# Optimization experiments

Measured on AMD Instinct MI355X. Metric: run time of the kernel, lower is better.

The kernel has to match this reference:

```python
import jax, jax.numpy as jnp
import numpy as np

N = 65536   # query points
M = 65536   # support points
H = 32      # neighbors per query
IN = 64     # input feature dim
OUT = 64    # out_dim // 2
K = 15      # kernel points
EXTENT = 0.1 * 1.2 / 2.5  # radius * kp_extent / conv_radius = 0.048
BN_EPS = 1e-5


def setup_inputs() -> dict:
    key = jax.random.key(0)
    ks = jax.random.split(key, 8)
    x = jax.random.normal(ks[0], (M, IN), dtype=jnp.float32)
    q_pts = jax.random.uniform(ks[1], (N, 3), dtype=jnp.float32) * 0.1
    s_pts = jax.random.uniform(ks[2], (M, 3), dtype=jnp.float32) * 0.1
    neighb_inds = jax.random.randint(ks[3], (N, H), 0, M, dtype=jnp.int32)
    kernel_points = jax.random.normal(ks[4], (K, 3), dtype=jnp.float32) * (0.5 * EXTENT)
    weights = jax.random.normal(ks[5], (K, IN, OUT), dtype=jnp.float32) * 0.05
    gamma = jnp.ones((OUT,), dtype=jnp.float32)
    beta = jnp.zeros((OUT,), dtype=jnp.float32)
    return {"x": x, "q_pts": q_pts, "s_pts": s_pts, "neighb_inds": neighb_inds,
            "kernel_points": kernel_points, "weights": weights,
            "gamma": gamma, "beta": beta}


def reference(x, q_pts, s_pts, neighb_inds, kernel_points, weights, gamma, beta):
    # --- KPConv (rigid, linear influence, sum aggregation) ---
    # Shadow point/feature for out-of-range neighbor indices (KPConv convention).
    s_pad = jnp.concatenate([s_pts, jnp.full((1, 3), 1e6, s_pts.dtype)], axis=0)
    x_pad = jnp.concatenate([x, jnp.zeros((1, x.shape[1]), x.dtype)], axis=0)

    # Relative neighbor coordinates: [N, H, 3]
    neighbors = s_pad[neighb_inds] - q_pts[:, None, :]
    # Squared distance to each kernel point: [N, H, K]
    diffs = neighbors[:, :, None, :] - kernel_points[None, None, :, :]
    sq_dist = jnp.sum(diffs * diffs, axis=-1)
    # Linear kernel-point influence, clipped at 0: [N, H, K]
    all_weights = jnp.maximum(1.0 - jnp.sqrt(sq_dist) / EXTENT, 0.0)

    # Gather neighbor features: [N, H, IN]
    neighb_x = x_pad[neighb_inds]
    # Influence-weighted aggregation per kernel point: [N, K, IN]
    weighted = jnp.einsum('nhk,nhi->nki', all_weights, neighb_x)
    # Apply per-kernel-point weight matrices and sum over kernel points: [N, OUT]
    out = jnp.einsum('nki,kio->no', weighted, weights)

    # --- BatchNorm (training-mode statistics over points) ---
    mean = jnp.mean(out, axis=0)
    var = jnp.var(out, axis=0)
    out = (out - mean) / jnp.sqrt(var + BN_EPS) * gamma + beta

    # --- LeakyReLU(0.1) ---
    return jnp.where(out >= 0, out, 0.1 * out)
```

## Files before the change

### kernel.cpp

```cpp
#include <hip/hip_runtime.h>
#include <math.h>

#define NQ   65536
#define H    32
#define IN   64
#define OUTC 64
#define K    15
#define QB   16
#define INV_EXT (1.0f / 0.048f)

#define OFF_PSUM  131072
#define OFF_SCSH  (OFF_PSUM + 2097152)
#define OFF_XBF   (OFF_SCSH + 1024)
#define NEED_BF16 (OFF_XBF + (size_t)NQ * IN * 2)

typedef __attribute__((ext_vector_type(8))) short short8;
typedef __attribute__((ext_vector_type(4))) short short4v;
typedef __attribute__((ext_vector_type(4))) float float4v;

static __device__ __forceinline__ unsigned short f2bf(float f) {
    return (unsigned short)((__float_as_uint(f) + 0x8000u) >> 16);
}
static __device__ __forceinline__ unsigned pk2(float a, float b) {
    return (__float_as_uint(a) + 0x8000u) >> 16 |
           ((__float_as_uint(b) + 0x8000u) & 0xFFFF0000u);
}

__global__ __launch_bounds__(256) void prep_all(
    const float* __restrict__ W, const float* __restrict__ x,
    short* __restrict__ Bfrag, unsigned short* __restrict__ xbf, int do_x)
{
    const int b = blockIdx.x;
    if (b < 4096) {
        if (do_x) {
            const int t = b * 256 + threadIdx.x;
            const float4 v = ((const float4*)x)[t];
            uint2 p; p.x = pk2(v.x, v.y); p.y = pk2(v.z, v.w);
            ((uint2*)xbf)[t] = p;
        }
    } else {
        const int t2  = (b - 4096) * 256 + threadIdx.x;
        const int j   = t2 & 7;
        const int ln  = (t2 >> 3) & 63;
        const int tt  = (t2 >> 9) & 31;
        const int wvq = t2 >> 14;
        const int kp2 = tt * 32 + (ln >> 4) * 8 + j;
        const int kq  = kp2 & 15;
        const int ii  = kp2 >> 4;
        const int oo  = wvq * 16 + (ln & 15);
        const float val = (kq < K) ? W[(kq * 64 + ii) * 64 + oo] : 0.0f;
        Bfrag[t2] = (short)f2bf(val);
    }
}

template<bool BFX>
__global__ __launch_bounds__(256, 5) void kpconv_mfma(
    const float* __restrict__ x, const unsigned short* __restrict__ xbf,
    const float* __restrict__ qp, const float* __restrict__ sp,
    const int* __restrict__ inds, const float* __restrict__ kp,
    const short* __restrict__ Bfrag, float* __restrict__ out_raw,
    float* __restrict__ psum)
{
    __shared__ __align__(16) short lds[16384];
    short* xn  = lds;
    short* wT2 = lds + 8448;

    const int tid  = threadIdx.x;
    const int lane = tid & 63;
    const int wv   = tid >> 6;
    const int quad = lane >> 4;
    const int ml   = lane & 15;
    const int q8   = lane >> 3;
    const int m8   = lane & 7;
    const int q0   = blockIdx.x * QB;

    short* xn_own = xn + wv * 2112;

    short8  xv[4][4];
    float4v xf[4][4][2];
#pragma unroll
    for (int qi = 0; qi < 4; ++qi) {
        const int ibase = (q0 + wv * 4 + qi) * H;
#pragma unroll
        for (int j = 0; j < 4; ++j) {
            const int id = inds[ibase + j * 8 + q8];
            if (BFX) {
                xv[qi][j] = *(const short8*)((const short*)xbf + id * IN + m8 * 8);
            } else {
                xf[qi][j][0] = *(const float4v*)(x + id * IN + m8 * 8);
                xf[qi][j][1] = *(const float4v*)(x + id * IN + m8 * 8 + 4);
            }
        }
    }

#pragma unroll
    for (int rep = 0; rep < 2; ++rep) {
        const int p  = lane + rep * 64;
        const int qi = p >> 5, h = p & 31;
        const int qg = wv * 4 + qi;
        const int n  = q0 + qg;
        const int id = inds[n * H + h];
        const float dx = sp[id * 3 + 0] - qp[n * 3 + 0];
        const float dy = sp[id * 3 + 1] - qp[n * 3 + 1];
        const float dz = sp[id * 3 + 2] - qp[n * 3 + 2];
        short8 w0, w1;
#pragma unroll
        for (int k = 0; k < K; ++k) {
            const float ex = dx - kp[k * 3 + 0];
            const float ey = dy - kp[k * 3 + 1];
            const float ez = dz - kp[k * 3 + 2];
            const float sq = ex * ex + ey * ey + ez * ez;
            float wval = 1.0f - __builtin_amdgcn_sqrtf(sq) * INV_EXT;
            wval = wval > 0.0f ? wval : 0.0f;
            if (k < 8) w0[k]     = (short)f2bf(wval);
            else       w1[k - 8] = (short)f2bf(wval);
        }
        w1[7] = 0;
        short* dst = wT2 + qg * 512 + ((h >> 2) & 1) * 256 + (h >> 3) * 64 + (h & 3) * 16;
        *(short8*)dst       = w0;
        *(short8*)(dst + 8) = w1;
    }

#pragma unroll
    for (int qi = 0; qi < 3; ++qi)
#pragma unroll
        for (int j = 0; j < 4; ++j) {
            if (BFX) {
                asm volatile("" :: "v"(xv[qi][j]));
            } else {
                asm volatile("" :: "v"(xf[qi][j][0]));
                asm volatile("" :: "v"(xf[qi][j][1]));
            }
        }

    const unsigned ldsb = (unsigned)(size_t)(&lds[0]);
    const unsigned xnb  = ldsb + (unsigned)(wv * 4224 + lane * 8);
    const unsigned wtb  = ldsb + 16896u + (unsigned)(wv * 4096 + lane * 8);

    float4v frag[4][4];
#pragma unroll
    for (int qi = 0; qi < 4; ++qi)
#pragma unroll
        for (int v = 0; v < 4; ++v) frag[qi][v] = (float4v){0.f, 0.f, 0.f, 0.f};

    const int Eb = (m8 >> 1) * 528 + ((q8 >> 2) & 1) * 256 + (q8 & 3) * 16 + (m8 & 1) * 8;

#pragma unroll
    for (int qi = 0; qi < 4; ++qi) {
#pragma unroll
        for (int j = 0; j < 4; ++j) {
            short8 pv;
            if (BFX) {
                pv = xv[qi][j];
            } else {
                const float4v a0 = xf[qi][j][0], a1 = xf[qi][j][1];
                pv[0] = (short)f2bf(a0[0]); pv[1] = (short)f2bf(a0[1]);
                pv[2] = (short)f2bf(a0[2]); pv[3] = (short)f2bf(a0[3]);
                pv[4] = (short)f2bf(a1[0]); pv[5] = (short)f2bf(a1[1]);
                pv[6] = (short)f2bf(a1[2]); pv[7] = (short)f2bf(a1[3]);
            }
            *(short8*)&xn_own[Eb + j * 64] = pv;
        }
        __builtin_amdgcn_sched_barrier(0);

        short4v a0, a1, b0[4], b1[4];
        asm volatile("ds_read_b64_tr_b16 %0, %1 offset:%c2"
                     : "=v"(a0) : "v"(wtb), "i"(qi * 1024) : "memory");
        asm volatile("ds_read_b64_tr_b16 %0, %1 offset:%c2"
                     : "=v"(a1) : "v"(wtb), "i"(qi * 1024 + 512) : "memory");
#pragma unroll
        for (int v = 0; v < 4; ++v) {
            asm volatile("ds_read_b64_tr_b16 %0, %1 offset:%c2"
                         : "=v"(b0[v]) : "v"(xnb), "i"(v * 1056) : "memory");
            asm volatile("ds_read_b64_tr_b16 %0, %1 offset:%c2"
                         : "=v"(b1[v]) : "v"(xnb), "i"(v * 1056 + 512) : "memory");
        }
        asm volatile("s_waitcnt lgkmcnt(0)");
        __builtin_amdgcn_sched_barrier(0);

        short8 a;
#pragma unroll
        for (int e = 0; e < 4; ++e) { a[e] = a0[e]; a[e + 4] = a1[e]; }
#pragma unroll
        for (int v = 0; v < 4; ++v) {
            short8 bb;
#pragma unroll
            for (int e = 0; e < 4; ++e) { bb[e] = b0[v][e]; bb[e + 4] = b1[v][e]; }
            frag[qi][v] = __builtin_amdgcn_mfma_f32_16x16x32_bf16(a, bb, frag[qi][v], 0, 0, 0);
        }
    }

    __syncthreads();

    char* AwtB = (char*)lds;
#pragma unroll
    for (int qi = 0; qi < 4; ++qi) {
        const int qg = wv * 4 + qi;
        char* qb = AwtB + qg * 2048;
        const int xr = ((qg & 7) << 4) ^ (((qg >> 3) & 1) << 3) ^ ((ml >> 2) << 3);
#pragma unroll
        for (int v = 0; v < 4; ++v) {
            short4v w;
#pragma unroll
            for (int r = 0; r < 4; ++r) w[r] = (short)f2bf(frag[qi][v][r]);
            const int Bw = (v * 16 + ml) * 32 + quad * 8;
            *(short4v*)(qb + (Bw ^ xr)) = w;
        }
    }
    __syncthreads();

    float4v acc0 = (float4v){0.f, 0.f, 0.f, 0.f};
    float4v acc1 = (float4v){0.f, 0.f, 0.f, 0.f};
    const short* bptr = Bfrag + (wv * 32) * 512 + lane * 8;
    const char*  arow = AwtB + ml * 2048;
    const int    xr2  = ((ml & 7) << 4) ^ (((ml >> 3) & 1) << 3);
#pragma unroll 2
    for (int t = 0; t < 32; t += 2) {
        {
            const int Br = t * 64 + quad * 16;
            const int ad = Br ^ xr2 ^ (((t >> 1) & 3) << 3);
            const short4v alo = *(const short4v*)(arow + ad);
            const short4v ahi = *(const short4v*)(arow + (ad ^ 8));
            short8 a;
#pragma unroll
            for (int e = 0; e < 4; ++e) { a[e] = alo[e]; a[e + 4] = ahi[e]; }
            const short8 bb = *(const short8*)(bptr + t * 512);
            acc0 = __builtin_amdgcn_mfma_f32_16x16x32_bf16(a, bb, acc0, 0, 0, 0);
        }
        {
            const int t1 = t + 1;
            const int Br = t1 * 64 + quad * 16;
            const int ad = Br ^ xr2 ^ (((t1 >> 1) & 3) << 3);
            const short4v alo = *(const short4v*)(arow + ad);
            const short4v ahi = *(const short4v*)(arow + (ad ^ 8));
            short8 a;
#pragma unroll
            for (int e = 0; e < 4; ++e) { a[e] = alo[e]; a[e + 4] = ahi[e]; }
            const short8 bb = *(const short8*)(bptr + t1 * 512);
            acc1 = __builtin_amdgcn_mfma_f32_16x16x32_bf16(a, bb, acc1, 0, 0, 0);
        }
    }
    const float4v acc = acc0 + acc1;

    float s = 0.f, s2 = 0.f;
#pragma unroll
    for (int r = 0; r < 4; ++r) {
        const float v = acc[r];
        out_raw[(q0 + quad * 4 + r) * OUTC + wv * 16 + ml] = v;
        s += v; s2 += v * v;
    }
    s  += __shfl_xor(s, 16, 64);  s  += __shfl_xor(s, 32, 64);
    s2 += __shfl_xor(s2, 16, 64); s2 += __shfl_xor(s2, 32, 64);
    if (quad == 0) {
        const int c = wv * 16 + ml;
        psum[c * 4096 + blockIdx.x]          = s;
        psum[262144 + c * 4096 + blockIdx.x] = s2;
    }
}

__global__ __launch_bounds__(256) void bn_stats(
    const float* __restrict__ psum, const float* __restrict__ gamma,
    const float* __restrict__ beta, float* __restrict__ sc_sh)
{
    const int c = blockIdx.x;
    const int t = threadIdx.x;
    float s = 0.f, q = 0.f;
#pragma unroll
    for (int i = 0; i < 16; ++i) {
        s += psum[c * 4096 + t + i * 256];
        q += psum[262144 + c * 4096 + t + i * 256];
    }
    __shared__ float rs[4], rq[4];
#pragma unroll
    for (int off = 32; off; off >>= 1) {
        s += __shfl_down(s, off, 64);
        q += __shfl_down(q, off, 64);
    }
    if ((t & 63) == 0) { rs[t >> 6] = s; rq[t >> 6] = q; }
    __syncthreads();
    if (t == 0) {
        s = rs[0] + rs[1] + rs[2] + rs[3];
        q = rq[0] + rq[1] + rq[2] + rq[3];
        const float mean = s * (1.0f / (float)NQ);
        const float var  = q * (1.0f / (float)NQ) - mean * mean;
        const float scale = gamma[c] / sqrtf(var + 1e-5f);
        sc_sh[c]      = scale;
        sc_sh[64 + c] = beta[c] - mean * scale;
    }
}

__global__ __launch_bounds__(256) void bn_apply(
    float* __restrict__ out, const float* __restrict__ sc_sh)
{
    __shared__ float sc[64];
    __shared__ float sh[64];
    if (threadIdx.x < 64) {
        sc[threadIdx.x] = sc_sh[threadIdx.x];
        sh[threadIdx.x] = sc_sh[64 + threadIdx.x];
    }
    __syncthreads();
    const int idx = blockIdx.x * 256 + threadIdx.x;
#pragma unroll
    for (int it = 0; it < 4; ++it) {
        const int e = idx + it * 262144;
        float4 v = ((const float4*)out)[e];
        const int cg = (e & 15) * 4;
        float4 r;
        r.x = v.x * sc[cg + 0] + sh[cg + 0];
        r.y = v.y * sc[cg + 1] + sh[cg + 1];
        r.z = v.z * sc[cg + 2] + sh[cg + 2];
        r.w = v.w * sc[cg + 3] + sh[cg + 3];
        r.x = r.x >= 0.0f ? r.x : 0.1f * r.x;
        r.y = r.y >= 0.0f ? r.y : 0.1f * r.y;
        r.z = r.z >= 0.0f ? r.z : 0.1f * r.z;
        r.w = r.w >= 0.0f ? r.w : 0.1f * r.w;
        ((float4*)out)[e] = r;
    }
}

extern "C" void kernel_launch(void* const* d_in, const int* in_sizes, int n_in,
                              void* d_out, int out_size, void* d_ws, size_t ws_size,
                              hipStream_t stream)
{
    (void)in_sizes; (void)n_in; (void)out_size;
    const float* x     = (const float*)d_in[0];
    const float* qp    = (const float*)d_in[1];
    const float* sp    = (const float*)d_in[2];
    const int*   inds  = (const int*)d_in[3];
    const float* kp    = (const float*)d_in[4];
    const float* W     = (const float*)d_in[5];
    const float* gamma = (const float*)d_in[6];
    const float* beta  = (const float*)d_in[7];
    float* out = (float*)d_out;

    short*          Bfrag = (short*)d_ws;
    float*          psum  = (float*)((char*)d_ws + OFF_PSUM);
    float*          sc_sh = (float*)((char*)d_ws + OFF_SCSH);
    unsigned short* xbf   = (unsigned short*)((char*)d_ws + OFF_XBF);

    const int use_bf = (ws_size >= NEED_BF16) ? 1 : 0;

    prep_all<<<4352, 256, 0, stream>>>(W, x, Bfrag, xbf, use_bf);
    if (use_bf)
        kpconv_mfma<true><<<NQ / QB, 256, 0, stream>>>(x, xbf, qp, sp, inds, kp, Bfrag, out, psum);
    else
        kpconv_mfma<false><<<NQ / QB, 256, 0, stream>>>(x, xbf, qp, sp, inds, kp, Bfrag, out, psum);
    bn_stats<<<64, 256, 0, stream>>>(psum, gamma, beta, sc_sh);
    bn_apply<<<1024, 256, 0, stream>>>(out, sc_sh);
}
```

Baseline: 145.5 us.

## Fuse prep, KPConv, BN stats and BN apply into one cooperative persistent kernel

Replaces the four-launch pipeline (prep, kpconv, bn_stats, bn_apply) with a single cooperative kernel. It runs the weight and feature prep, grid-syncs, loops persistently over query tiles accumulating per-thread BN sums, reduces them with atomics, grid-syncs again and then applies BN plus LeakyReLU. The goal is to remove launch gaps and the separate partial-sum pass. The costs are grid-wide barriers, a persistent grid limited by occupancy with fewer blocks than tiles, and atomic float accumulation of the statistics. If the cooperative launch fails, the code falls back to the old path.

New measurement: 366.2 us. 152% more time.

```diff
diff --git a/kernel.cpp b/kernel.cpp
--- a/kernel.cpp
+++ b/kernel.cpp
@@ -1,5 +1,8 @@
 #include <hip/hip_runtime.h>
+#include <hip/hip_cooperative_groups.h>
 #include <math.h>
+
+namespace cg = cooperative_groups;
 
 #define NQ   65536
 #define H    32
@@ -7,6 +10,7 @@
 #define OUTC 64
 #define K    15
 #define QB   16
+#define NTILE 4096
 #define INV_EXT (1.0f / 0.048f)
 
 #define OFF_PSUM  131072
@@ -24,6 +28,271 @@
 static __device__ __forceinline__ unsigned pk2(float a, float b) {
     return (__float_as_uint(a) + 0x8000u) >> 16 |
            ((__float_as_uint(b) + 0x8000u) & 0xFFFF0000u);
+}
+
+template<bool BFX>
+__global__ __launch_bounds__(256, 4) void kpconv_fused(
+    const float* __restrict__ x, unsigned short* __restrict__ xbf,
+    const float* __restrict__ qp, const float* __restrict__ sp,
+    const int* __restrict__ inds, const float* __restrict__ kp,
+    short* __restrict__ Bfrag, const float* __restrict__ W,
+    const float* __restrict__ gamma, const float* __restrict__ beta,
+    float* __restrict__ out, float* __restrict__ gsum)
+{
+    __shared__ __align__(16) short lds[16384];
+    short* xn  = lds;
+    short* wT2 = lds + 8448;
+
+    const int tid  = threadIdx.x;
+    const int lane = tid & 63;
+    const int wv   = tid >> 6;
+    const int quad = lane >> 4;
+    const int ml   = lane & 15;
+    const int q8   = lane >> 3;
+    const int m8   = lane & 7;
+    const int G    = gridDim.x;
+
+    if (blockIdx.x < 256) {
+        const int t2  = blockIdx.x * 256 + tid;
+        const int j   = t2 & 7;
+        const int ln  = (t2 >> 3) & 63;
+        const int tt  = (t2 >> 9) & 31;
+        const int wvq = t2 >> 14;
+        const int kp2 = tt * 32 + (ln >> 4) * 8 + j;
+        const int kq  = kp2 & 15;
+        const int ii  = kp2 >> 4;
+        const int oo  = wvq * 16 + (ln & 15);
+        const float val = (kq < K) ? W[(kq * 64 + ii) * 64 + oo] : 0.0f;
+        Bfrag[t2] = (short)f2bf(val);
+    }
+    if (BFX) {
+        for (unsigned t = blockIdx.x * 256u + tid; t < 1048576u; t += (unsigned)G * 256u) {
+            const float4 v = ((const float4*)x)[t];
+            uint2 p; p.x = pk2(v.x, v.y); p.y = pk2(v.z, v.w);
+            ((uint2*)xbf)[t] = p;
+        }
+    }
+    if (blockIdx.x == 0 && tid < 128) gsum[tid] = 0.0f;
+    __threadfence();
+    cg::this_grid().sync();
+
+    short* xn_own = xn + wv * 2112;
+    const unsigned ldsb = (unsigned)(size_t)(&lds[0]);
+    const unsigned xnb  = ldsb + (unsigned)(wv * 4224 + lane * 8);
+    const unsigned wtb  = ldsb + 16896u + (unsigned)(wv * 4096 + lane * 8);
+    const int hbase_q8  = q8;
+    const int Eb = (m8 >> 1) * 528 + ((q8 >> 2) & 1) * 256 + (q8 & 3) * 16 + (m8 & 1) * 8;
+
+    float s_tot = 0.0f, s2_tot = 0.0f;
+
+    for (int tile = blockIdx.x; tile < NTILE; tile += G) {
+        const int q0 = tile * QB;
+
+        short8  xv[4][4];
+        float4v xf[4][4][2];
+#pragma unroll
+        for (int qi = 0; qi < 4; ++qi) {
+            const int ibase = (q0 + wv * 4 + qi) * H;
+#pragma unroll
+            for (int j = 0; j < 4; ++j) {
+                const int id = inds[ibase + j * 8 + hbase_q8];
+                if (BFX) {
+                    xv[qi][j] = *(const short8*)((const short*)xbf + id * IN + m8 * 8);
+                } else {
+                    xf[qi][j][0] = *(const float4v*)(x + id * IN + m8 * 8);
+                    xf[qi][j][1] = *(const float4v*)(x + id * IN + m8 * 8 + 4);
+                }
+            }
+        }
+
+#pragma unroll
+        for (int rep = 0; rep < 2; ++rep) {
+            const int p  = lane + rep * 64;
+            const int qi = p >> 5, h = p & 31;
+            const int qg = wv * 4 + qi;
+            const int n  = q0 + qg;
+            const int id = inds[n * H + h];
+            const float dx = sp[id * 3 + 0] - qp[n * 3 + 0];
+            const float dy = sp[id * 3 + 1] - qp[n * 3 + 1];
+            const float dz = sp[id * 3 + 2] - qp[n * 3 + 2];
+            short8 w0, w1;
+#pragma unroll
+            for (int k = 0; k < K; ++k) {
+                const float ex = dx - kp[k * 3 + 0];
+                const float ey = dy - kp[k * 3 + 1];
+                const float ez = dz - kp[k * 3 + 2];
+                const float sq = ex * ex + ey * ey + ez * ez;
+                float wval = 1.0f - __builtin_amdgcn_sqrtf(sq) * INV_EXT;
+                wval = wval > 0.0f ? wval : 0.0f;
+                if (k < 8) w0[k]     = (short)f2bf(wval);
+                else       w1[k - 8] = (short)f2bf(wval);
+            }
+            w1[7] = 0;
+            short* dst = wT2 + qg * 512 + ((h >> 2) & 1) * 256 + (h >> 3) * 64 + (h & 3) * 16;
+            *(short8*)dst       = w0;
+            *(short8*)(dst + 8) = w1;
+        }
+
+#pragma unroll
+        for (int qi = 0; qi < 3; ++qi)
+#pragma unroll
+            for (int j = 0; j < 4; ++j) {
+                if (BFX) {
+                    asm volatile("" :: "v"(xv[qi][j]));
+                } else {
+                    asm volatile("" :: "v"(xf[qi][j][0]));
+                    asm volatile("" :: "v"(xf[qi][j][1]));
+                }
+            }
+
+        float4v frag[4][4];
+#pragma unroll
+        for (int qi = 0; qi < 4; ++qi)
+#pragma unroll
+            for (int v = 0; v < 4; ++v) frag[qi][v] = (float4v){0.f, 0.f, 0.f, 0.f};
+
+#pragma unroll
+        for (int qi = 0; qi < 4; ++qi) {
+#pragma unroll
+            for (int j = 0; j < 4; ++j) {
+                short8 pv;
+                if (BFX) {
+                    pv = xv[qi][j];
+                } else {
+                    const float4v a0 = xf[qi][j][0], a1 = xf[qi][j][1];
+                    pv[0] = (short)f2bf(a0[0]); pv[1] = (short)f2bf(a0[1]);
+                    pv[2] = (short)f2bf(a0[2]); pv[3] = (short)f2bf(a0[3]);
+                    pv[4] = (short)f2bf(a1[0]); pv[5] = (short)f2bf(a1[1]);
+                    pv[6] = (short)f2bf(a1[2]); pv[7] = (short)f2bf(a1[3]);
+                }
+                *(short8*)&xn_own[Eb + j * 64] = pv;
+            }
+            __builtin_amdgcn_sched_barrier(0);
+
+            short4v a0, a1, b0[4], b1[4];
+            asm volatile("ds_read_b64_tr_b16 %0, %1 offset:%c2"
+                         : "=v"(a0) : "v"(wtb), "i"(qi * 1024) : "memory");
+            asm volatile("ds_read_b64_tr_b16 %0, %1 offset:%c2"
+                         : "=v"(a1) : "v"(wtb), "i"(qi * 1024 + 512) : "memory");
+#pragma unroll
+            for (int v = 0; v < 4; ++v) {
+                asm volatile("ds_read_b64_tr_b16 %0, %1 offset:%c2"
+                             : "=v"(b0[v]) : "v"(xnb), "i"(v * 1056) : "memory");
+                asm volatile("ds_read_b64_tr_b16 %0, %1 offset:%c2"
+                             : "=v"(b1[v]) : "v"(xnb), "i"(v * 1056 + 512) : "memory");
+            }
+            asm volatile("s_waitcnt lgkmcnt(0)");
+            __builtin_amdgcn_sched_barrier(0);
+
+            short8 a;
+#pragma unroll
+            for (int e = 0; e < 4; ++e) { a[e] = a0[e]; a[e + 4] = a1[e]; }
+#pragma unroll
+            for (int v = 0; v < 4; ++v) {
+                short8 bb;
+#pragma unroll
+                for (int e = 0; e < 4; ++e) { bb[e] = b0[v][e]; bb[e + 4] = b1[v][e]; }
+                frag[qi][v] = __builtin_amdgcn_mfma_f32_16x16x32_bf16(a, bb, frag[qi][v], 0, 0, 0);
+            }
+        }
+
+        __syncthreads();
+
+        char* AwtB = (char*)lds;
+#pragma unroll
+        for (int qi = 0; qi < 4; ++qi) {
+            const int qg = wv * 4 + qi;
+            char* qb = AwtB + qg * 2048;
+            const int xr = ((qg & 7) << 4) ^ (((qg >> 3) & 1) << 3) ^ ((ml >> 2) << 3);
+#pragma unroll
+            for (int v = 0; v < 4; ++v) {
+                short4v w;
+#pragma unroll
+                for (int r = 0; r < 4; ++r) w[r] = (short)f2bf(frag[qi][v][r]);
+                const int Bw = (v * 16 + ml) * 32 + quad * 8;
+                *(short4v*)(qb + (Bw ^ xr)) = w;
+            }
+        }
+        __syncthreads();
+
+        float4v acc0 = (float4v){0.f, 0.f, 0.f, 0.f};
+        float4v acc1 = (float4v){0.f, 0.f, 0.f, 0.f};
+        const short* bptr = Bfrag + (wv * 32) * 512 + lane * 8;
+        const char*  arow = AwtB + ml * 2048;
+        const int    xr2  = ((ml & 7) << 4) ^ (((ml >> 3) & 1) << 3);
+#pragma unroll 2
+        for (int t = 0; t < 32; t += 2) {
+            {
+                const int Br = t * 64 + quad * 16;
+                const int ad = Br ^ xr2 ^ (((t >> 1) & 3) << 3);
+                const short4v alo = *(const short4v*)(arow + ad);
+                const short4v ahi = *(const short4v*)(arow + (ad ^ 8));
+                short8 a;
+#pragma unroll
+                for (int e = 0; e < 4; ++e) { a[e] = alo[e]; a[e + 4] = ahi[e]; }
+                const short8 bb = *(const short8*)(bptr + t * 512);
+                acc0 = __builtin_amdgcn_mfma_f32_16x16x32_bf16(a, bb, acc0, 0, 0, 0);
+            }
+            {
+                const int t1 = t + 1;
+                const int Br = t1 * 64 + quad * 16;
+                const int ad = Br ^ xr2 ^ (((t1 >> 1) & 3) << 3);
+                const short4v alo = *(const short4v*)(arow + ad);
+                const short4v ahi = *(const short4v*)(arow + (ad ^ 8));
+                short8 a;
+#pragma unroll
+                for (int e = 0; e < 4; ++e) { a[e] = alo[e]; a[e + 4] = ahi[e]; }
+                const short8 bb = *(const short8*)(bptr + t1 * 512);
+                acc1 = __builtin_amdgcn_mfma_f32_16x16x32_bf16(a, bb, acc1, 0, 0, 0);
+            }
+        }
+        const float4v acc = acc0 + acc1;
+
+#pragma unroll
+        for (int r = 0; r < 4; ++r) {
+            const float v = acc[r];
+            out[(q0 + quad * 4 + r) * OUTC + wv * 16 + ml] = v;
+            s_tot  += v;
+            s2_tot += v * v;
+        }
+        __syncthreads();
+    }
+
+    s_tot  += __shfl_xor(s_tot, 16, 64);  s_tot  += __shfl_xor(s_tot, 32, 64);
+    s2_tot += __shfl_xor(s2_tot, 16, 64); s2_tot += __shfl_xor(s2_tot, 32, 64);
+    if (quad == 0) {
+        const int c = wv * 16 + ml;
+        atomicAdd(&gsum[c], s_tot);
+        atomicAdd(&gsum[64 + c], s2_tot);
+    }
+    __threadfence();
+    cg::this_grid().sync();
+
+    float* scf = (float*)lds;
+    float* shf = scf + 64;
+    if (tid < 64) {
+        const float S = gsum[tid], Q = gsum[64 + tid];
+        const float mean = S * (1.0f / (float)NQ);
+        const float var  = Q * (1.0f / (float)NQ) - mean * mean;
+        const float scale = gamma[tid] / sqrtf(var + 1e-5f);
+        scf[tid] = scale;
+        shf[tid] = beta[tid] - mean * scale;
+    }
+    __syncthreads();
+    for (unsigned e = blockIdx.x * 256u + tid; e < 1048576u; e += (unsigned)G * 256u) {
+        float4 v = ((const float4*)out)[e];
+        const int cgi = (e & 15) * 4;
+        float4 r;
+        r.x = v.x * scf[cgi + 0] + shf[cgi + 0];
+        r.y = v.y * scf[cgi + 1] + shf[cgi + 1];
+        r.z = v.z * scf[cgi + 2] + shf[cgi + 2];
+        r.w = v.w * scf[cgi + 3] + shf[cgi + 3];
+        r.x = r.x >= 0.0f ? r.x : 0.1f * r.x;
+        r.y = r.y >= 0.0f ? r.y : 0.1f * r.y;
+        r.z = r.z >= 0.0f ? r.z : 0.1f * r.z;
+        r.w = r.w >= 0.0f ? r.w : 0.1f * r.w;
+        ((float4*)out)[e] = r;
+    }
 }
 
 __global__ __launch_bounds__(256) void prep_all(
@@ -335,16 +604,44 @@
 
     short*          Bfrag = (short*)d_ws;
     float*          psum  = (float*)((char*)d_ws + OFF_PSUM);
-    float*          sc_sh = (float*)((char*)d_ws + OFF_SCSH);
+    float*          gsum  = (float*)((char*)d_ws + OFF_SCSH);
     unsigned short* xbf   = (unsigned short*)((char*)d_ws + OFF_XBF);
 
     const int use_bf = (ws_size >= NEED_BF16) ? 1 : 0;
 
-    prep_all<<<4352, 256, 0, stream>>>(W, x, Bfrag, xbf, use_bf);
+    int nb = 0;
+    hipError_t qerr;
     if (use_bf)
-        kpconv_mfma<true><<<NQ / QB, 256, 0, stream>>>(x, xbf, qp, sp, inds, kp, Bfrag, out, psum);
+        qerr = hipOccupancyMaxActiveBlocksPerMultiprocessor(&nb, kpconv_fused<true>, 256, 0);
     else
-        kpconv_mfma<false><<<NQ / QB, 256, 0, stream>>>(x, xbf, qp, sp, inds, kp, Bfrag, out, psum);
-    bn_stats<<<64, 256, 0, stream>>>(psum, gamma, beta, sc_sh);
-    bn_apply<<<1024, 256, 0, stream>>>(out, sc_sh);
-}
+        qerr = hipOccupancyMaxActiveBlocksPerMultiprocessor(&nb, kpconv_fused<false>, 256, 0);
+    if (qerr != hipSuccess || nb < 1) nb = 1;
+    int grid = nb * 256;
+    if (grid > NTILE) grid = NTILE;
+    if (grid < 256) grid = 256;
+
+    void* args[12];
+    args[0]  = (void*)&x;     args[1]  = (void*)&xbf;
+    args[2]  = (void*)&qp;    args[3]  = (void*)&sp;
+    args[4]  = (void*)&inds;  args[5]  = (void*)&kp;
+    args[6]  = (void*)&Bfrag; args[7]  = (void*)&W;
+    args[8]  = (void*)&gamma; args[9]  = (void*)&beta;
+    args[10] = (void*)&out;   args[11] = (void*)&gsum;
+
+    hipError_t lerr;
+    if (use_bf)
+        lerr = hipLaunchCooperativeKernel(kpconv_fused<true>,  dim3(grid), dim3(256), args, 0, stream);
+    else
+        lerr = hipLaunchCooperativeKernel(kpconv_fused<false>, dim3(grid), dim3(256), args, 0, stream);
+
+    if (lerr != hipSuccess) {
+        (void)hipGetLastError();
+        prep_all<<<4352, 256, 0, stream>>>(W, x, Bfrag, xbf, use_bf);
+        if (use_bf)
+            kpconv_mfma<true><<<NQ / QB, 256, 0, stream>>>(x, xbf, qp, sp, inds, kp, Bfrag, out, psum);
+        else
+            kpconv_mfma<false><<<NQ / QB, 256, 0, stream>>>(x, xbf, qp, sp, inds, kp, Bfrag, out, psum);
+        bn_stats<<<64, 256, 0, stream>>>(psum, gamma, beta, gsum);
+        bn_apply<<<1024, 256, 0, stream>>>(out, gsum);
+    }
+}
```
